# Kernel tuning notes

Hardware: AMD Instinct MI355X
Metric: run time of the kernel (lower is better)

## Reference

```python
import jax, jax.numpy as jnp
import numpy as np

TOKENS = 8192
D_IN = 4096
D_OUT = 4096


def setup_inputs() -> dict:
    key = jax.random.key(0)
    k1, k2, k3 = jax.random.split(key, 3)
    input = jax.random.normal(k1, (TOKENS, D_IN), dtype=jnp.float32)
    # int8 quantized weight, stored here as int32 (stand-in for torch.int8 buffer)
    weight = jax.random.randint(k2, (D_OUT, D_IN), -127, 127, dtype=jnp.int32)
    # per-output-channel dequant scales
    scales = jax.random.uniform(k3, (D_OUT,), dtype=jnp.float32) * 0.02
    return {"input": input, "weight": weight, "scales": scales}


def reference(input, weight, scales):
    # F.linear(input, weight.to(input.dtype), bias=False) * scales
    w = weight.astype(input.dtype)            # dequantize to input dtype
    out = jnp.einsum('ti,oi->to', input, w)   # [tokens, out_features]
    return out * scales.astype(input.dtype)   # per-channel scale
```

## Files before the change

### kernel.cpp

```cpp
#include <hip/hip_runtime.h>
#include <hip/hip_bf16.h>

typedef __bf16 bf16;
typedef __bf16 bf16x8 __attribute__((ext_vector_type(8)));
typedef float  f32x4  __attribute__((ext_vector_type(4)));

#define M_DIM 8192
#define N_DIM 4096
#define K_DIM 4096
#define NT    (K_DIM / 64)

#define GLOBAL_AS __attribute__((address_space(1)))
#define LDS_AS    __attribute__((address_space(3)))


__global__ __launch_bounds__(256) void cvt_input_bf16(const float4* __restrict__ in,
                                                      bf16x8* __restrict__ out) {
    int idx = blockIdx.x * 256 + threadIdx.x;
    float4 v0 = in[2 * idx];
    float4 v1 = in[2 * idx + 1];
    bf16x8 o;
    o[0] = (bf16)v0.x; o[1] = (bf16)v0.y; o[2] = (bf16)v0.z; o[3] = (bf16)v0.w;
    o[4] = (bf16)v1.x; o[5] = (bf16)v1.y; o[6] = (bf16)v1.z; o[7] = (bf16)v1.w;
    out[idx] = o;
}

__global__ __launch_bounds__(256) void cvt_weight_bf16(const int4* __restrict__ in,
                                                       bf16x8* __restrict__ out) {
    int idx = blockIdx.x * 256 + threadIdx.x;
    int4 v0 = in[2 * idx];
    int4 v1 = in[2 * idx + 1];
    bf16x8 o;
    o[0] = (bf16)(float)v0.x; o[1] = (bf16)(float)v0.y;
    o[2] = (bf16)(float)v0.z; o[3] = (bf16)(float)v0.w;
    o[4] = (bf16)(float)v1.x; o[5] = (bf16)(float)v1.y;
    o[6] = (bf16)(float)v1.z; o[7] = (bf16)(float)v1.w;
    out[idx] = o;
}


__global__ __launch_bounds__(512, 2) void gemm_bt_256(const bf16* __restrict__ A,
                                                      const bf16* __restrict__ B,
                                                      const float* __restrict__ scales,
                                                      float* __restrict__ C) {
    __shared__ bf16 ldsA[2 * 16384];
    __shared__ bf16 ldsB[2 * 16384];

    const int tid  = threadIdx.x;
    const int wave = tid >> 6;
    const int lane = tid & 63;
    const int wm   = wave >> 2;
    const int wn   = wave & 3;

    const int wg = blockIdx.x;
    const int x  = wg & 7;
    const int c  = wg >> 3;
    const int m0 = ((x & 1) * 16 + (c >> 2)) * 256;
    const int n0 = ((x >> 1) * 4 + (c & 3)) * 256;

    const int sr = tid >> 3;
    const int sc = ((tid & 7) ^ (sr & 7)) * 8;
    const int so = tid * 8;

    const int la15 = lane & 15;
    const int lhi  = lane >> 4;
    const int rlow = la15 & 7;
    const int ck0  = ((lhi) ^ rlow) * 8;
    const int ck1  = ((4 + lhi) ^ rlow) * 8;
    const int wrA  = wm * 128;
    const int wrB  = wn * 64;

    f32x4  acc[8][4] = {};
    bf16x8 afA[4], afB[4], bA[4], bB[4];

#define STAGE_A(KT, H) do {                                                              \
    const int _kk = (KT) & (NT - 1);                                                     \
    const int _bb = ((KT) & 1) * 16384;                                                  \
    const bf16* _g0 = A + (size_t)(m0 + (H) * 128 + sr) * K_DIM + _kk * 64 + sc;         \
    __builtin_amdgcn_global_load_lds((GLOBAL_AS const void*)_g0,                         \
        (LDS_AS void*)(ldsA + _bb + (H) * 8192 + so), 16, 0, 0);                         \
    const bf16* _g1 = A + (size_t)(m0 + (H) * 128 + 64 + sr) * K_DIM + _kk * 64 + sc;    \
    __builtin_amdgcn_global_load_lds((GLOBAL_AS const void*)_g1,                         \
        (LDS_AS void*)(ldsA + _bb + (H) * 8192 + 4096 + so), 16, 0, 0);                  \
} while (0)

#define STAGE_B(KT, H) do {                                                              \
    const int _kk = (KT) & (NT - 1);                                                     \
    const int _bb = ((KT) & 1) * 16384;                                                  \
    const bf16* _g0 = B + (size_t)(n0 + (H) * 128 + sr) * K_DIM + _kk * 64 + sc;         \
    __builtin_amdgcn_global_load_lds((GLOBAL_AS const void*)_g0,                         \
        (LDS_AS void*)(ldsB + _bb + (H) * 8192 + so), 16, 0, 0);                         \
    const bf16* _g1 = B + (size_t)(n0 + (H) * 128 + 64 + sr) * K_DIM + _kk * 64 + sc;    \
    __builtin_amdgcn_global_load_lds((GLOBAL_AS const void*)_g1,                         \
        (LDS_AS void*)(ldsB + _bb + (H) * 8192 + 4096 + so), 16, 0, 0);                  \
} while (0)

#define LD_A(MH, KH, DST, BO) do {                                                       \
    _Pragma("unroll")                                                                    \
    for (int _i = 0; _i < 4; ++_i) {                                                     \
        const int _r = (BO) + (wrA + (MH) * 64 + _i * 16 + la15) * 64;                   \
        DST[_i] = *(const bf16x8*)(ldsA + _r + ((KH) ? ck1 : ck0));                      \
    }                                                                                    \
} while (0)

#define LD_B(KH, DST, BO) do {                                                           \
    _Pragma("unroll")                                                                    \
    for (int _j = 0; _j < 4; ++_j) {                                                     \
        const int _r = (BO) + (wrB + _j * 16 + la15) * 64;                               \
        DST[_j] = *(const bf16x8*)(ldsB + _r + ((KH) ? ck1 : ck0));                      \
    }                                                                                    \
} while (0)

#define MMA_Q(I0, AF, BF) do {                                                           \
    __builtin_amdgcn_s_setprio(1);                                                       \
    _Pragma("unroll")                                                                    \
    for (int _i = 0; _i < 4; ++_i) {                                                     \
        _Pragma("unroll")                                                                \
        for (int _j = 0; _j < 4; ++_j) {                                                 \
            acc[(I0) + _i][_j] = __builtin_amdgcn_mfma_f32_16x16x32_bf16(                \
                AF[_i], BF[_j], acc[(I0) + _i][_j], 0, 0, 0);                            \
        }                                                                                \
    }                                                                                    \
    __builtin_amdgcn_s_setprio(0);                                                       \
} while (0)

#define BAR() __builtin_amdgcn_s_barrier()

    STAGE_A(0, 0); STAGE_B(0, 0); STAGE_A(0, 1); STAGE_B(0, 1);
    STAGE_B(1, 0); STAGE_A(1, 0);
    asm volatile("s_waitcnt vmcnt(4)" ::: "memory");
    BAR();
    LD_A(0, 0, afA, 0);
    LD_B(0, bA, 0);

    for (int t = 0; t < NT; ++t) {
        const int bo = (t & 1) * 16384;
        const int bn = bo ^ 16384;

        STAGE_A(t + 1, 1);
        LD_A(1, 0, afB, bo);
        MMA_Q(0, afA, bA);
        BAR();

        STAGE_B(t + 1, 1);
        LD_A(1, 1, afA, bo);
        LD_B(1, bB, bo);
        MMA_Q(4, afB, bA);
        BAR();

        STAGE_B(t + 2, 0);
        LD_A(0, 1, afB, bo);
        MMA_Q(4, afA, bB);
        BAR();

        STAGE_A(t + 2, 0);
        asm volatile("s_waitcnt vmcnt(4)" ::: "memory");
        BAR();
        LD_A(0, 0, afA, bn);
        LD_B(0, bA, bn);
        MMA_Q(0, afB, bB);
        BAR();
    }

    asm volatile("s_waitcnt vmcnt(0)" ::: "memory");

    const int crow = lhi * 4;
#pragma unroll
    for (int j = 0; j < 4; ++j) {
        const int col = n0 + wrB + j * 16 + la15;
        const float s = scales[col];
#pragma unroll
        for (int i = 0; i < 8; ++i) {
            const int rowb = m0 + wrA + i * 16 + crow;
#pragma unroll
            for (int r = 0; r < 4; ++r)
                C[(size_t)(rowb + r) * N_DIM + col] = acc[i][j][r] * s;
        }
    }

#undef STAGE_A
#undef STAGE_B
#undef LD_A
#undef LD_B
#undef MMA_Q
#undef BAR
}


__global__ __launch_bounds__(256, 2) void gemm_fused(const float* __restrict__ A,
                                                     const int* __restrict__ B,
                                                     const float* __restrict__ scales,
                                                     float* __restrict__ C) {
    __shared__ bf16 lds_a[128 * 32];
    __shared__ bf16 lds_b[128 * 32];

    const int tid  = threadIdx.x;
    const int wave = tid >> 6;
    const int lane = tid & 63;
    const int m0 = blockIdx.y * 128;
    const int n0 = blockIdx.x * 128;
    const int wm = (wave >> 1) * 64;
    const int wn = (wave & 1) * 64;

    const int sr = tid >> 1;
    const int sc = (tid & 1) * 16;

    const int la = lane & 15;
    const int lk = (lane >> 4) * 8;

    f32x4 acc[4][4] = {};

    for (int k0 = 0; k0 < K_DIM; k0 += 32) {
        __syncthreads();
        {
            const float* ga = A + (size_t)(m0 + sr) * K_DIM + k0 + sc;
            float4 v0 = *(const float4*)(ga + 0);
            float4 v1 = *(const float4*)(ga + 4);
            float4 v2 = *(const float4*)(ga + 8);
            float4 v3 = *(const float4*)(ga + 12);
            bf16x8 p0, p1;
            p0[0]=(bf16)v0.x; p0[1]=(bf16)v0.y; p0[2]=(bf16)v0.z; p0[3]=(bf16)v0.w;
            p0[4]=(bf16)v1.x; p0[5]=(bf16)v1.y; p0[6]=(bf16)v1.z; p0[7]=(bf16)v1.w;
            p1[0]=(bf16)v2.x; p1[1]=(bf16)v2.y; p1[2]=(bf16)v2.z; p1[3]=(bf16)v2.w;
            p1[4]=(bf16)v3.x; p1[5]=(bf16)v3.y; p1[6]=(bf16)v3.z; p1[7]=(bf16)v3.w;
            *(bf16x8*)(lds_a + sr * 32 + sc)     = p0;
            *(bf16x8*)(lds_a + sr * 32 + sc + 8) = p1;
        }
        {
            const int* gb = B + (size_t)(n0 + sr) * K_DIM + k0 + sc;
            int4 v0 = *(const int4*)(gb + 0);
            int4 v1 = *(const int4*)(gb + 4);
            int4 v2 = *(const int4*)(gb + 8);
            int4 v3 = *(const int4*)(gb + 12);
            bf16x8 p0, p1;
            p0[0]=(bf16)(float)v0.x; p0[1]=(bf16)(float)v0.y; p0[2]=(bf16)(float)v0.z; p0[3]=(bf16)(float)v0.w;
            p0[4]=(bf16)(float)v1.x; p0[5]=(bf16)(float)v1.y; p0[6]=(bf16)(float)v1.z; p0[7]=(bf16)(float)v1.w;
            p1[0]=(bf16)(float)v2.x; p1[1]=(bf16)(float)v2.y; p1[2]=(bf16)(float)v2.z; p1[3]=(bf16)(float)v2.w;
            p1[4]=(bf16)(float)v3.x; p1[5]=(bf16)(float)v3.y; p1[6]=(bf16)(float)v3.z; p1[7]=(bf16)(float)v3.w;
            *(bf16x8*)(lds_b + sr * 32 + sc)     = p0;
            *(bf16x8*)(lds_b + sr * 32 + sc + 8) = p1;
        }
        __syncthreads();

        bf16x8 af[4], bfg[4];
#pragma unroll
        for (int i = 0; i < 4; ++i)
            af[i] = *(const bf16x8*)(lds_a + (wm + i * 16 + la) * 32 + lk);
#pragma unroll
        for (int j = 0; j < 4; ++j)
            bfg[j] = *(const bf16x8*)(lds_b + (wn + j * 16 + la) * 32 + lk);
#pragma unroll
        for (int i = 0; i < 4; ++i)
#pragma unroll
            for (int j = 0; j < 4; ++j)
                acc[i][j] = __builtin_amdgcn_mfma_f32_16x16x32_bf16(af[i], bfg[j], acc[i][j], 0, 0, 0);
    }

    const int crow = (lane >> 4) * 4;
#pragma unroll
    for (int j = 0; j < 4; ++j) {
        const int col = n0 + wn + j * 16 + la;
        const float s = scales[col];
#pragma unroll
        for (int i = 0; i < 4; ++i) {
            const int rowb = m0 + wm + i * 16 + crow;
#pragma unroll
            for (int r = 0; r < 4; ++r)
                C[(size_t)(rowb + r) * N_DIM + col] = acc[i][j][r] * s;
        }
    }
}


extern "C" void kernel_launch(void* const* d_in, const int* in_sizes, int n_in,
                              void* d_out, int out_size, void* d_ws, size_t ws_size,
                              hipStream_t stream) {
    const float* input  = (const float*)d_in[0];
    const int*   weight = (const int*)d_in[1];
    const float* scales = (const float*)d_in[2];
    float* out = (float*)d_out;

    const size_t needA = (size_t)M_DIM * K_DIM * sizeof(bf16);
    const size_t needB = (size_t)N_DIM * K_DIM * sizeof(bf16);

    if (ws_size >= needA + needB) {
        bf16* Abf = (bf16*)d_ws;
        bf16* Bbf = (bf16*)((char*)d_ws + needA);
        cvt_input_bf16<<<(M_DIM * (size_t)K_DIM / 8) / 256, 256, 0, stream>>>(
            (const float4*)input, (bf16x8*)Abf);
        cvt_weight_bf16<<<(N_DIM * (size_t)K_DIM / 8) / 256, 256, 0, stream>>>(
            (const int4*)weight, (bf16x8*)Bbf);
        gemm_bt_256<<<(M_DIM / 256) * (N_DIM / 256), 512, 0, stream>>>(Abf, Bbf, scales, out);
    } else {
        dim3 grid(N_DIM / 128, M_DIM / 128);
        gemm_fused<<<grid, 256, 0, stream>>>(input, weight, scales, out);
    }
}
```

Before: 623.9 us.

## Switch GEMM to 32x32x16 MFMA tiles and fuse conversion kernels

Result: faster. 548.6 us (-12.1%).

```diff
diff --git a/kernel.cpp b/kernel.cpp
--- a/kernel.cpp
+++ b/kernel.cpp
@@ -3,6 +3,7 @@
 
 typedef __bf16 bf16;
 typedef __bf16 bf16x8 __attribute__((ext_vector_type(8)));
+typedef float  f32x16 __attribute__((ext_vector_type(16)));
 typedef float  f32x4  __attribute__((ext_vector_type(4)));
 
 #define M_DIM 8192
@@ -14,28 +15,33 @@
 #define LDS_AS    __attribute__((address_space(3)))
 
 
-__global__ __launch_bounds__(256) void cvt_input_bf16(const float4* __restrict__ in,
-                                                      bf16x8* __restrict__ out) {
-    int idx = blockIdx.x * 256 + threadIdx.x;
-    float4 v0 = in[2 * idx];
-    float4 v1 = in[2 * idx + 1];
-    bf16x8 o;
-    o[0] = (bf16)v0.x; o[1] = (bf16)v0.y; o[2] = (bf16)v0.z; o[3] = (bf16)v0.w;
-    o[4] = (bf16)v1.x; o[5] = (bf16)v1.y; o[6] = (bf16)v1.z; o[7] = (bf16)v1.w;
-    out[idx] = o;
-}
-
-__global__ __launch_bounds__(256) void cvt_weight_bf16(const int4* __restrict__ in,
-                                                       bf16x8* __restrict__ out) {
-    int idx = blockIdx.x * 256 + threadIdx.x;
-    int4 v0 = in[2 * idx];
-    int4 v1 = in[2 * idx + 1];
-    bf16x8 o;
-    o[0] = (bf16)(float)v0.x; o[1] = (bf16)(float)v0.y;
-    o[2] = (bf16)(float)v0.z; o[3] = (bf16)(float)v0.w;
-    o[4] = (bf16)(float)v1.x; o[5] = (bf16)(float)v1.y;
-    o[6] = (bf16)(float)v1.z; o[7] = (bf16)(float)v1.w;
-    out[idx] = o;
+#define CVT_A_BLOCKS 16384
+#define CVT_B_BLOCKS 8192
+
+__global__ __launch_bounds__(256) void cvt_both(const float4* __restrict__ a_in,
+                                                bf16x8* __restrict__ a_out,
+                                                const int4* __restrict__ b_in,
+                                                bf16x8* __restrict__ b_out) {
+    const int b = blockIdx.x;
+    if (b < CVT_A_BLOCKS) {
+        int idx = b * 256 + threadIdx.x;
+        float4 v0 = a_in[2 * idx];
+        float4 v1 = a_in[2 * idx + 1];
+        bf16x8 o;
+        o[0] = (bf16)v0.x; o[1] = (bf16)v0.y; o[2] = (bf16)v0.z; o[3] = (bf16)v0.w;
+        o[4] = (bf16)v1.x; o[5] = (bf16)v1.y; o[6] = (bf16)v1.z; o[7] = (bf16)v1.w;
+        a_out[idx] = o;
+    } else {
+        int idx = (b - CVT_A_BLOCKS) * 256 + threadIdx.x;
+        int4 v0 = b_in[2 * idx];
+        int4 v1 = b_in[2 * idx + 1];
+        bf16x8 o;
+        o[0] = (bf16)(float)v0.x; o[1] = (bf16)(float)v0.y;
+        o[2] = (bf16)(float)v0.z; o[3] = (bf16)(float)v0.w;
+        o[4] = (bf16)(float)v1.x; o[5] = (bf16)(float)v1.y;
+        o[6] = (bf16)(float)v1.z; o[7] = (bf16)(float)v1.w;
+        b_out[idx] = o;
+    }
 }
 
 
@@ -62,16 +68,18 @@
     const int sc = ((tid & 7) ^ (sr & 7)) * 8;
     const int so = tid * 8;
 
-    const int la15 = lane & 15;
-    const int lhi  = lane >> 4;
-    const int rlow = la15 & 7;
-    const int ck0  = ((lhi) ^ rlow) * 8;
-    const int ck1  = ((4 + lhi) ^ rlow) * 8;
-    const int wrA  = wm * 128;
-    const int wrB  = wn * 64;
-
-    f32x4  acc[8][4] = {};
-    bf16x8 afA[4], afB[4], bA[4], bB[4];
+    const int l31 = lane & 31;
+    const int hi2 = lane >> 5;
+    const int r7  = l31 & 7;
+    int cks[4];
+#pragma unroll
+    for (int ks = 0; ks < 4; ++ks) cks[ks] = ((ks * 2 + hi2) ^ r7) * 8;
+
+    const int wrA = wm * 128;
+    const int wrB = wn * 64;
+
+    f32x16 acc[4][2] = {};
+    bf16x8 af[2][4], bf0[4], bf1[4];
 
 #define STAGE_A(KT, H) do {                                                              \
     const int _kk = (KT) & (NT - 1);                                                     \
@@ -95,30 +103,31 @@
         (LDS_AS void*)(ldsB + _bb + (H) * 8192 + 4096 + so), 16, 0, 0);                  \
 } while (0)
 
-#define LD_A(MH, KH, DST, BO) do {                                                       \
+#define LD_A(MH, BO) do {                                                                \
     _Pragma("unroll")                                                                    \
-    for (int _i = 0; _i < 4; ++_i) {                                                     \
-        const int _r = (BO) + (wrA + (MH) * 64 + _i * 16 + la15) * 64;                   \
-        DST[_i] = *(const bf16x8*)(ldsA + _r + ((KH) ? ck1 : ck0));                      \
+    for (int _mf = 0; _mf < 2; ++_mf) {                                                  \
+        const int _row = wrA + (MH) * 64 + _mf * 32 + l31;                               \
+        _Pragma("unroll")                                                                \
+        for (int _ks = 0; _ks < 4; ++_ks)                                                \
+            af[_mf][_ks] = *(const bf16x8*)(ldsA + (BO) + _row * 64 + cks[_ks]);         \
     }                                                                                    \
 } while (0)
 
-#define LD_B(KH, DST, BO) do {                                                           \
+#define LD_B(NH, DST, BO) do {                                                           \
+    const int _row = wrB + (NH) * 32 + l31;                                              \
     _Pragma("unroll")                                                                    \
-    for (int _j = 0; _j < 4; ++_j) {                                                     \
-        const int _r = (BO) + (wrB + _j * 16 + la15) * 64;                               \
-        DST[_j] = *(const bf16x8*)(ldsB + _r + ((KH) ? ck1 : ck0));                      \
-    }                                                                                    \
-} while (0)
-
-#define MMA_Q(I0, AF, BF) do {                                                           \
+    for (int _ks = 0; _ks < 4; ++_ks)                                                    \
+        DST[_ks] = *(const bf16x8*)(ldsB + (BO) + _row * 64 + cks[_ks]);                 \
+} while (0)
+
+#define MMA_Q(MH, NH, BF) do {                                                           \
     __builtin_amdgcn_s_setprio(1);                                                       \
     _Pragma("unroll")                                                                    \
-    for (int _i = 0; _i < 4; ++_i) {                                                     \
+    for (int _ks = 0; _ks < 4; ++_ks) {                                                  \
         _Pragma("unroll")                                                                \
-        for (int _j = 0; _j < 4; ++_j) {                                                 \
-            acc[(I0) + _i][_j] = __builtin_amdgcn_mfma_f32_16x16x32_bf16(                \
-                AF[_i], BF[_j], acc[(I0) + _i][_j], 0, 0, 0);                            \
+        for (int _mf = 0; _mf < 2; ++_mf) {                                              \
+            acc[(MH) * 2 + _mf][NH] = __builtin_amdgcn_mfma_f32_32x32x16_bf16(           \
+                af[_mf][_ks], BF[_ks], acc[(MH) * 2 + _mf][NH], 0, 0, 0);                \
         }                                                                                \
     }                                                                                    \
     __builtin_amdgcn_s_setprio(0);                                                       \
@@ -130,51 +139,50 @@
     STAGE_B(1, 0); STAGE_A(1, 0);
     asm volatile("s_waitcnt vmcnt(4)" ::: "memory");
     BAR();
-    LD_A(0, 0, afA, 0);
-    LD_B(0, bA, 0);
 
     for (int t = 0; t < NT; ++t) {
         const int bo = (t & 1) * 16384;
-        const int bn = bo ^ 16384;
-
+
+        LD_A(0, bo);
+        LD_B(0, bf0, bo);
         STAGE_A(t + 1, 1);
-        LD_A(1, 0, afB, bo);
-        MMA_Q(0, afA, bA);
-        BAR();
-
+        BAR();
+        MMA_Q(0, 0, bf0);
+        BAR();
+
+        LD_B(1, bf1, bo);
         STAGE_B(t + 1, 1);
-        LD_A(1, 1, afA, bo);
-        LD_B(1, bB, bo);
-        MMA_Q(4, afB, bA);
-        BAR();
-
+        BAR();
+        MMA_Q(0, 1, bf1);
+        BAR();
+
+        LD_A(1, bo);
         STAGE_B(t + 2, 0);
-        LD_A(0, 1, afB, bo);
-        MMA_Q(4, afA, bB);
+        BAR();
+        MMA_Q(1, 1, bf1);
         BAR();
 
         STAGE_A(t + 2, 0);
+        BAR();
+        MMA_Q(1, 0, bf0);
         asm volatile("s_waitcnt vmcnt(4)" ::: "memory");
         BAR();
-        LD_A(0, 0, afA, bn);
-        LD_B(0, bA, bn);
-        MMA_Q(0, afB, bB);
-        BAR();
     }
 
     asm volatile("s_waitcnt vmcnt(0)" ::: "memory");
 
-    const int crow = lhi * 4;
-#pragma unroll
-    for (int j = 0; j < 4; ++j) {
-        const int col = n0 + wrB + j * 16 + la15;
+#pragma unroll
+    for (int g = 0; g < 2; ++g) {
+        const int col = n0 + wrB + g * 32 + l31;
         const float s = scales[col];
 #pragma unroll
-        for (int i = 0; i < 8; ++i) {
-            const int rowb = m0 + wrA + i * 16 + crow;
-#pragma unroll
-            for (int r = 0; r < 4; ++r)
-                C[(size_t)(rowb + r) * N_DIM + col] = acc[i][j][r] * s;
+        for (int f = 0; f < 4; ++f) {
+            const int mbase = m0 + wrA + f * 32 + 4 * hi2;
+#pragma unroll
+            for (int r = 0; r < 16; ++r) {
+                const int row = mbase + (r & 3) + 8 * (r >> 2);
+                C[(size_t)row * N_DIM + col] = acc[f][g][r] * s;
+            }
         }
     }
 
@@ -286,10 +294,8 @@
     if (ws_size >= needA + needB) {
         bf16* Abf = (bf16*)d_ws;
         bf16* Bbf = (bf16*)((char*)d_ws + needA);
-        cvt_input_bf16<<<(M_DIM * (size_t)K_DIM / 8) / 256, 256, 0, stream>>>(
-            (const float4*)input, (bf16x8*)Abf);
-        cvt_weight_bf16<<<(N_DIM * (size_t)K_DIM / 8) / 256, 256, 0, stream>>>(
-            (const int4*)weight, (bf16x8*)Bbf);
+        cvt_both<<<CVT_A_BLOCKS + CVT_B_BLOCKS, 256, 0, stream>>>(
+            (const float4*)input, (bf16x8*)Abf, (const int4*)weight, (bf16x8*)Bbf);
         gemm_bt_256<<<(M_DIM / 256) * (N_DIM / 256), 512, 0, stream>>>(Abf, Bbf, scales, out);
     } else {
         dim3 grid(N_DIM / 128, M_DIM / 128);
```
